# Kernel tuning notes

Hardware: AMD Instinct MI355X
Metric: run time of the kernel (lower is better)

## Reference

```python
import jax, jax.numpy as jnp
import numpy as np

B, C, D, H, W = 2, 180, 16, 32, 32
NH, WS, I = 6, 8, 2
HD = C // NH
SCALE = HD ** -0.5
N = WS ** 3                      # 512 tokens per window
TABLE = (2 * WS - 1) ** 3        # 3375 relative-position entries
HID = int(C * 4.0)               # MLP hidden
CR = C // 3                      # CAB compressed channels (compress_ratio=3)
SQ = C // 30                     # channel-attn squeeze (squeeze_factor=30)
CONV_SCALE = 0.01
EPS = 1e-5


def layer_norm(x, g, b):
    m = jnp.mean(x, axis=-1, keepdims=True)
    v = jnp.mean((x - m) ** 2, axis=-1, keepdims=True)
    return (x - m) * jax.lax.rsqrt(v + EPS) * g + b


def setup_inputs() -> dict:
    key = jax.random.key(0)
    ks = jax.random.split(key, 12)
    n = lambda i, shape: jax.random.normal(ks[i], shape, jnp.float32) * 0.02
    return {
        "x": jax.random.normal(ks[0], (B, D * H * W, C), jnp.float32),
        "x_size_d": D, "x_size_h": H, "x_size_w": W,
        "rpi_sa": jax.random.randint(ks[1], (N, N), 0, TABLE),
        "attn_mask": jnp.zeros((1,), jnp.float32),
        "triangular_masks": jnp.zeros((1,), jnp.float32),
        "g1": jnp.ones((C,), jnp.float32), "b1": jnp.zeros((C,), jnp.float32),
        "qkv_w": n(2, (3 * C, C)), "qkv_b": jnp.zeros((3 * C,), jnp.float32),
        "rpb": n(3, (TABLE, NH)),
        "proj_w": n(4, (C, C)), "proj_b": jnp.zeros((C,), jnp.float32),
        "cw1": n(5, (CR, C, 3, 3, 3)), "cb1": jnp.zeros((CR,), jnp.float32),
        "cw2": n(6, (C, CR, 3, 3, 3)), "cb2": jnp.zeros((C,), jnp.float32),
        "caw1": n(7, (SQ, C)), "cab1": jnp.zeros((SQ,), jnp.float32),
        "caw2": n(8, (C, SQ)), "cab2": jnp.zeros((C,), jnp.float32),
        "g2": jnp.ones((C,), jnp.float32), "b2": jnp.zeros((C,), jnp.float32),
        "fc1_w": n(9, (HID, C)), "fc1_b": jnp.zeros((HID,), jnp.float32),
        "fc2_w": n(10, (C, HID)), "fc2_b": jnp.zeros((C,), jnp.float32),
    }


def reference(x, x_size_d, x_size_h, x_size_w, rpi_sa, attn_mask, triangular_masks,
              g1, b1, qkv_w, qkv_b, rpb, proj_w, proj_b,
              cw1, cb1, cw2, cb2, caw1, cab1, caw2, cab2,
              g2, b2, fc1_w, fc1_b, fc2_w, fc2_b):
    Dd, Hd, Wd = x_size_d, x_size_h, x_size_w
    shortcut = x
    xn = layer_norm(x, g1, b1).reshape(B, Dd, Hd, Wd, C)

    # ---- CAB conv branch (conv3 -> gelu -> conv3 -> channel attention) ----
    xc = jnp.transpose(xn, (0, 4, 1, 2, 3))  # B C D H W
    dn = ("NCDHW", "OIDHW", "NCDHW")
    y = jax.lax.conv_general_dilated(xc, cw1, (1, 1, 1), "SAME", dimension_numbers=dn)
    y = jax.nn.gelu(y + cb1[None, :, None, None, None], approximate=False)
    y = jax.lax.conv_general_dilated(y, cw2, (1, 1, 1), "SAME", dimension_numbers=dn)
    y = y + cb2[None, :, None, None, None]
    pooled = jnp.mean(y, axis=(2, 3, 4))                      # B C (AdaptiveAvgPool3d(1))
    a = jax.nn.relu(pooled @ caw1.T + cab1)
    a = jax.nn.sigmoid(a @ caw2.T + cab2)                     # B C
    y = y * a[:, :, None, None, None]
    conv_x = jnp.transpose(y, (0, 2, 3, 4, 1)).reshape(B, Dd * Hd * Wd, C)

    # ---- sparse interval partition (interval=2, no pad, no shift) ----
    Gd, Gh, Gw = Dd // I, Hd // I, Wd // I
    xs = xn.reshape(B, Gd, I, Gh, I, Gw, I, C)
    xs = jnp.transpose(xs, (0, 2, 4, 6, 1, 3, 5, 7)).reshape(B * I ** 3, Gd, Gh, Gw, C)

    # ---- 3D window partition ----
    nd, nh, nw = Gd // WS, Gh // WS, Gw // WS
    xw = xs.reshape(-1, nd, WS, nh, WS, nw, WS, C)
    xw = jnp.transpose(xw, (0, 1, 3, 5, 2, 4, 6, 7)).reshape(-1, N, C)

    # ---- window attention with relative-position bias ----
    qkv = (xw @ qkv_w.T + qkv_b).reshape(-1, N, 3, NH, HD)
    qkv = jnp.transpose(qkv, (2, 0, 3, 1, 4))                 # 3, nWin, NH, N, HD
    q, k, v = qkv[0] * SCALE, qkv[1], qkv[2]
    attn = jnp.einsum("whnd,whmd->whnm", q, k)
    bias = rpb[rpi_sa.reshape(-1)].reshape(N, N, NH)
    attn = jax.nn.softmax(attn + jnp.transpose(bias, (2, 0, 1))[None], axis=-1)
    out = jnp.einsum("whnm,whmd->whnd", attn, v)
    out = jnp.transpose(out, (0, 2, 1, 3)).reshape(-1, N, C)
    out = out @ proj_w.T + proj_b

    # ---- window reverse + sparse reverse ----
    xs = out.reshape(-1, nd, nh, nw, WS, WS, WS, C)
    xs = jnp.transpose(xs, (0, 1, 4, 2, 5, 3, 6, 7)).reshape(B * I ** 3, Gd, Gh, Gw, C)
    xs = xs.reshape(B, I, I, I, Gd, Gh, Gw, C)
    xs = jnp.transpose(xs, (0, 4, 1, 5, 2, 6, 3, 7)).reshape(B, Dd, Hd, Wd, C)
    attn_x = xs.reshape(B, Dd * Hd * Wd, C)

    # ---- residual + conv branch, then MLP ----
    x = shortcut + attn_x + conv_x * CONV_SCALE
    h = layer_norm(x, g2, b2)
    h = jax.nn.gelu(h @ fc1_w.T + fc1_b, approximate=False) @ fc2_w.T + fc2_b
    return x + h
```

## Files before the change

### kernel.cpp

```cpp
#include <hip/hip_runtime.h>
#include <math.h>

static constexpr int CCH = 180;
static constexpr float SCALE_Q = 0.18257418583505536f;

typedef short short8 __attribute__((ext_vector_type(8)));
typedef float f32x4 __attribute__((ext_vector_type(4)));

static constexpr size_t OFF_ATTNB = 0;
static constexpr size_t OFF_XNP   = 3145728;
static constexpr size_t OFF_Y1P   = 7140864;
static constexpr size_t OFF_QKVB  = 8472576;
static constexpr size_t OFF_HID   = 0;
static constexpr size_t OFF_Y2B   = 17909760;
static constexpr size_t OFF_X2    = 21055488;
static constexpr size_t OFF_X2N   = 26953728;
static constexpr size_t OFF_BIASB = 30099456;
static constexpr size_t OFF_WQKV  = 30885888;
static constexpr size_t OFF_WPROJ = 30947328;
static constexpr size_t OFF_WFC1  = 30971904;
static constexpr size_t OFF_WFC2  = 31045632;
static constexpr size_t OFF_WB1   = 31143936;
static constexpr size_t OFF_WB2   = 31309824;
static constexpr size_t OFF_PPART = 31475712;
static constexpr size_t OFF_POOL  = 31487232;
static constexpr size_t OFF_AM    = 31487592;

__device__ __forceinline__ float geluf(float v){
  return 0.5f*v*(1.0f + erff(v*0.70710678118654752440f));
}
__device__ __forceinline__ short f2bf(float f){
  unsigned u = __float_as_uint(f);
  unsigned r = (u + 0x7FFFu + ((u>>16)&1u)) >> 16;
  return (short)r;
}
__device__ __forceinline__ float bf2f(short s){
  return __uint_as_float(((unsigned)(unsigned short)s)<<16);
}
__device__ __forceinline__ void gload16(const void* g, void* l){
  __builtin_amdgcn_global_load_lds(
    (const __attribute__((address_space(1))) unsigned int*)g,
    (__attribute__((address_space(3))) unsigned int*)l, 16, 0, 0);
}

__global__ void prep_wb(const float* __restrict__ qkv_w, const float* __restrict__ proj_w,
                        const float* __restrict__ fc1_w, const float* __restrict__ fc2_w,
                        short* __restrict__ wq, short* __restrict__ wp,
                        short* __restrict__ w1, short* __restrict__ w2){
  int i = blockIdx.x*256 + threadIdx.x;
  if(i < 122880){
    int o = i/192, k = i - o*192;
    wq[i] = (o<540 && k<180) ? f2bf(qkv_w[o*180+k]) : (short)0;
  } else if(i < 172032){
    int j = i-122880; int o = j/192, k = j - o*192;
    wp[j] = (o<180 && k<180) ? f2bf(proj_w[o*180+k]) : (short)0;
  } else if(i < 319488){
    int j = i-172032; int o = j/192, k = j - o*192;
    w1[j] = (o<720 && k<180) ? f2bf(fc1_w[o*180+k]) : (short)0;
  } else if(i < 516096){
    int j = i-319488; int o = j/768, k = j - o*768;
    w2[j] = (o<180 && k<720) ? f2bf(fc2_w[o*720+k]) : (short)0;
  }
}

__global__ void prep_wbc(const float* __restrict__ cw1, const float* __restrict__ cw2,
                         short* __restrict__ wb1, short* __restrict__ wb2){
  int i = blockIdx.x*256 + threadIdx.x;
  if(i < 27*64*192){
    int t = i/(64*192); int rem = i - t*64*192;
    int co = rem/192, ci = rem - co*192;
    wb1[i] = (co<60 && ci<180) ? f2bf(cw1[(co*180+ci)*27 + t]) : (short)0;
    int co2 = rem/64, ci2 = rem - co2*64;
    wb2[i] = (co2<180 && ci2<60) ? f2bf(cw2[(co2*60+ci2)*27 + t]) : (short)0;
  }
}

__global__ __launch_bounds__(256) void bias_prep(const int* __restrict__ rpi,
    const float* __restrict__ rpb, short* __restrict__ biasB){
  int i = blockIdx.x*256 + threadIdx.x;
  int q = i>>9, k = i&511;
  int kt = k>>5, kin = k&31;
  int j = kt*32 + ((kin<16) ? 2*kin : 2*(kin-16)+1);
  int idx = rpi[i];
  #pragma unroll
  for(int h=0;h<6;h++)
    biasB[((size_t)h*512 + q)*512 + j] = f2bf(rpb[idx*6+h]);
}

template<int PADDED>
__global__ __launch_bounds__(256) void ln_bf16(const float* __restrict__ x,
    const float* __restrict__ g, const float* __restrict__ b, short* __restrict__ outb){
  int token = blockIdx.x*4 + (threadIdx.x>>6);
  int lane  = threadIdx.x & 63;
  const float* row = x + (size_t)token*CCH;
  float v0 = row[lane], v1 = row[lane+64];
  float v2 = (lane<52) ? row[lane+128] : 0.f;
  float s = v0+v1+v2;
  #pragma unroll
  for(int m=1;m<64;m<<=1) s += __shfl_xor(s, m, 64);
  float mean = s*(1.f/180.f);
  float d0=v0-mean, d1=v1-mean, d2=(lane<52)?(v2-mean):0.f;
  float sq = d0*d0+d1*d1+d2*d2;
  #pragma unroll
  for(int m=1;m<64;m<<=1) sq += __shfl_xor(sq, m, 64);
  float rstd = rsqrtf(sq*(1.f/180.f)+1e-5f);
  size_t orow;
  if(PADDED){
    int bb=token>>14, d=(token>>10)&15, h=(token>>5)&31, w=token&31;
    orow = ((size_t)((bb*18+d+1)*34 + h+1)*34 + w+1)*192;
  } else {
    orow = (size_t)token*192;
  }
  short* o = outb + orow;
  o[lane]    = f2bf(d0*rstd*g[lane]    + b[lane]);
  o[lane+64] = f2bf(d1*rstd*g[lane+64] + b[lane+64]);
  o[lane+128]= (lane<52) ? f2bf(d2*rstd*g[lane+128] + b[lane+128]) : (short)0;
}

__global__ __launch_bounds__(256) void conv1_mfma(const short* __restrict__ in,
    const short* __restrict__ wb, const float* __restrict__ cbias, short* __restrict__ y1p){
  __shared__ short lds[26112];
  int bid = blockIdx.x;
  int xcd = bid&7, idx = bid>>3;
  int b = idx>>5, dd=(idx>>4)&1, hg=idx&15;
  int d = xcd*2+dd;
  int h0 = hg*2;
  int tid=threadIdx.x, l=tid&63, l15=l&15, g=l>>4, wid=tid>>6;
  int soff[13];
  #pragma unroll
  for(int it=0; it<13; it++){
    int t = it*256 + tid;
    int rr = t/24, s = t - rr*24;
    soff[it] = rr*192 + (((s&~7)|((s&7)^(rr&7)))<<3);
  }
  f32x4 acc[4];
  #pragma unroll
  for(int mi=0;mi<4;mi++) acc[mi]=(f32x4){0.f,0.f,0.f,0.f};
  for(int kd=0;kd<3;kd++){
    {
      const short* S = in + (((size_t)(b*18+d+kd)*34 + h0)*34)*192;
      #pragma unroll
      for(int it=0; it<13; it++){
        if(it<12 || tid<192)
          gload16(S + soff[it], &lds[(it*256 + wid*64)*8]);
      }
    }
    __syncthreads();
    #pragma unroll
    for(int kh=0;kh<3;kh++)
    #pragma unroll
    for(int kw=0;kw<3;kw++){
      const short* wt = wb + (size_t)((kd*3+kh)*3+kw)*12288 + (wid*16+l15)*192;
      #pragma unroll
      for(int ks=0;ks<6;ks++){
        int s = ks*4+g;
        short8 bv = *(const short8*)&wt[ks*32 + g*8];
        #pragma unroll
        for(int mi=0;mi<4;mi++){
          int R = ((mi>>1)+kh)*34 + (mi&1)*16 + l15 + kw;
          short8 av = *(const short8*)&lds[R*192 + (((s&~7)|((s&7)^(R&7)))<<3)];
          acc[mi] = __builtin_amdgcn_mfma_f32_16x16x32_bf16(av, bv, acc[mi],0,0,0);
        }
      }
    }
    __syncthreads();
  }
  int co = wid*16+l15;
  float bb = (co<60)? cbias[co] : 0.f;
  #pragma unroll
  for(int mi=0;mi<4;mi++){
    int hr = mi>>1;
    #pragma unroll
    for(int reg=0;reg<4;reg++){
      int r = mi*16 + g*4 + reg;
      int w = r&31;
      y1p[(((size_t)(b*18+d+1)*34 + h0+hr+1)*34 + w+1)*64 + co] = f2bf(geluf(acc[mi][reg] + bb));
    }
  }
}

__global__ __launch_bounds__(256) void conv2_mfma(const short* __restrict__ in,
    const short* __restrict__ wb, const float* __restrict__ cbias, short* __restrict__ y2b){
  __shared__ short lds[8704];
  int bid = blockIdx.x;
  int xcd = bid&7, idx = bid>>3;
  int b = idx>>5, dd=(idx>>4)&1, hg=idx&15;
  int d = xcd*2+dd;
  int h0 = hg*2;
  int tid=threadIdx.x, l=tid&63, l15=l&15, g=l>>4, wid=tid>>6;
  int soff[5];
  #pragma unroll
  for(int it=0; it<5; it++){
    int t = it*256 + tid;
    int rr = t>>3, s = t&7;
    soff[it] = rr*64 + ((s^(rr&7))<<3);
  }
  f32x4 acc[4][3];
  #pragma unroll
  for(int mi=0;mi<4;mi++)
    #pragma unroll
    for(int nj=0;nj<3;nj++) acc[mi][nj]=(f32x4){0.f,0.f,0.f,0.f};
  for(int kd=0;kd<3;kd++){
    {
      const short* S = in + (((size_t)(b*18+d+kd)*34 + h0)*34)*64;
      #pragma unroll
      for(int it=0; it<5; it++){
        if(it<4 || tid<64)
          gload16(S + soff[it], &lds[(it*256 + wid*64)*8]);
      }
    }
    __syncthreads();
    #pragma unroll
    for(int kh=0;kh<3;kh++)
    #pragma unroll
    for(int kw=0;kw<3;kw++){
      const short* wt = wb + (size_t)((kd*3+kh)*3+kw)*12288;
      #pragma unroll
      for(int ks=0;ks<2;ks++){
        int s = ks*4+g;
        short8 bv[3];
        #pragma unroll
        for(int nj=0;nj<3;nj++)
          bv[nj] = *(const short8*)&wt[(size_t)(wid*48+nj*16+l15)*64 + ks*32 + g*8];
        #pragma unroll
        for(int mi=0;mi<4;mi++){
          int R = ((mi>>1)+kh)*34 + (mi&1)*16 + l15 + kw;
          short8 av = *(const short8*)&lds[R*64 + ((s^(R&7))<<3)];
          #pragma unroll
          for(int nj=0;nj<3;nj++)
            acc[mi][nj] = __builtin_amdgcn_mfma_f32_16x16x32_bf16(av, bv[nj], acc[mi][nj],0,0,0);
        }
      }
    }
    __syncthreads();
  }
  #pragma unroll
  for(int nj=0;nj<3;nj++){
    int co = wid*48 + nj*16 + l15;
    if(co<180){
      float bb = cbias[co];
      #pragma unroll
      for(int mi=0;mi<4;mi++){
        int hr = mi>>1;
        #pragma unroll
        for(int reg=0;reg<4;reg++){
          int r = mi*16 + g*4 + reg;
          int w = r&31;
          size_t token = ((size_t)(b*16+d)*32 + h0+hr)*32 + w;
          y2b[token*192 + co] = f2bf(acc[mi][nj][reg] + bb);
        }
      }
    }
  }
}

__global__ __launch_bounds__(192) void pool1_kernel(const short* __restrict__ y2b,
                                                    float* __restrict__ part){
  int b = blockIdx.x>>5, chunk = blockIdx.x&31;
  int c = threadIdx.x;
  if(c<180){
    float s = 0.f;
    const short* base = y2b + ((size_t)b*16384 + chunk*512)*192 + c;
    for(int it=0;it<512;it++) s += bf2f(base[(size_t)it*192]);
    part[blockIdx.x*180 + c] = s;
  }
}
__global__ void pool2_kernel(const float* __restrict__ part, float* __restrict__ pooled){
  int i = blockIdx.x*256 + threadIdx.x;
  if(i<360){
    int b = i/180, c = i - b*180;
    float s = 0.f;
    for(int ch=0;ch<32;ch++) s += part[(b*32+ch)*180 + c];
    pooled[i] = s*(1.f/16384.f);
  }
}

__global__ void chattn_kernel(const float* __restrict__ pooled,
    const float* __restrict__ caw1, const float* __restrict__ cab1,
    const float* __restrict__ caw2, const float* __restrict__ cab2,
    float* __restrict__ amask){
  __shared__ float hid[2][6];
  int t = threadIdx.x;
  if(t<12){
    int b = t/6, qh = t - b*6;
    float s = cab1[qh];
    for(int c=0;c<180;c++) s += pooled[b*180+c]*caw1[qh*180+c];
    hid[b][qh] = fmaxf(s, 0.f);
  }
  __syncthreads();
  for(int i=t;i<360;i+=64){
    int b = i/180, c = i - b*180;
    float s = cab2[c];
    #pragma unroll
    for(int qh=0;qh<6;qh++) s += hid[b][qh]*caw2[c*6+qh];
    amask[i] = 1.f/(1.f+__expf(-s));
  }
}

__device__ __forceinline__ void wtok_decomp(int t, int& b, int& dd, int& hh, int& ww){
  int win = t >> 9, n = t & 511;
  int sb = win >> 2, wi = win & 3;
  int wh = wi >> 1, wwi = wi & 1;
  b = sb >> 3; int r = sb & 7;
  int id = r >> 2, ih = (r>>1)&1, iw = r&1;
  int td = n >> 6, th = (n>>3)&7, tw = n & 7;
  dd = td*2 + id;
  hh = (wh*8+th)*2 + ih;
  ww = (wwi*8+tw)*2 + iw;
}
__device__ __forceinline__ int wtok_to_row(int t){
  int b,dd,hh,ww; wtok_decomp(t,b,dd,hh,ww);
  return b*16384 + (dd*32+hh)*32 + ww;
}
__device__ __forceinline__ int wtok_to_prow(int t){
  int b,dd,hh,ww; wtok_decomp(t,b,dd,hh,ww);
  return ((b*18+dd+1)*34 + hh+1)*34 + ww + 1;
}

template<int MODE, int NOUT, int KTOT>
__global__ __launch_bounds__(256) void mgemm(const short* __restrict__ A,
    const short* __restrict__ Wb, const float* __restrict__ bias, void* __restrict__ outv,
    const float* __restrict__ e0, const float* __restrict__ e1,
    const float* __restrict__ e2){
  __shared__ short As[2][8192];
  __shared__ short Bs[2][8192];
  __shared__ int rowmap[128];
  int lin = blockIdx.y*gridDim.x + blockIdx.x;
  int xcd = lin&7, k = lin>>3;
  int bm = xcd*32 + (k & 31);
  int bn = k >> 5;
  int tid = threadIdx.x;
  int l = tid&63, l15=l&15, g=l>>4, wid=tid>>6;
  int wm = wid>>1, wn = wid&1;
  constexpr int RS = (MODE==3)?768:192;
  if(MODE==0 || MODE==1){
    if(tid<128) rowmap[tid] = (MODE==0) ? wtok_to_prow(bm*128+tid) : wtok_to_row(bm*128+tid);
  }
  __syncthreads();
  f32x4 acc[4][4];
  #pragma unroll
  for(int i=0;i<4;i++)
    #pragma unroll
    for(int j=0;j<4;j++) acc[i][j] = (f32x4){0.f,0.f,0.f,0.f};

  constexpr int NCH = KTOT/64;
  auto STAGE = [&](int ch, int p){
    int k0 = ch*64;
    #pragma unroll
    for(int it=0; it<4; it++){
      int i = it*256 + wid*64 + l;
      int r = i>>3, sl = (i&7) ^ (r&7);
      size_t row = (size_t)((MODE==0||MODE==1) ? rowmap[r] : bm*128+r);
      gload16(A + row*RS + k0 + sl*8, &As[p][(size_t)(it*256+wid*64)*8]);
    }
    #pragma unroll
    for(int it=0; it<4; it++){
      int i = it*256 + wid*64 + l;
      int c = i>>3, sl = (i&7) ^ (c&7);
      gload16(Wb + (size_t)(bn*128+c)*KTOT + k0 + sl*8, &Bs[p][(size_t)(it*256+wid*64)*8]);
    }
  };
  STAGE(0,0);
  for(int ch=0; ch<NCH; ch++){
    if(ch+1<NCH){
      STAGE(ch+1,(ch+1)&1);
      asm volatile("s_waitcnt vmcnt(8)" ::: "memory");
    } else {
      asm volatile("s_waitcnt vmcnt(0)" ::: "memory");
    }
    __builtin_amdgcn_s_barrier();
    const short* as = As[ch&1];
    const short* bs = Bs[ch&1];
    #pragma unroll
    for(int ks=0; ks<2; ks++){
      short8 av[4], bv[4];
      #pragma unroll
      for(int i=0;i<4;i++){
        int r = wm*64 + i*16 + l15;
        av[i] = *(const short8*)&as[r*64 + (((ks*4+g) ^ (r&7))<<3)];
      }
      #pragma unroll
      for(int j=0;j<4;j++){
        int c = wn*64 + j*16 + l15;
        bv[j] = *(const short8*)&bs[c*64 + (((ks*4+g) ^ (c&7))<<3)];
      }
      #pragma unroll
      for(int i=0;i<4;i++)
        #pragma unroll
        for(int j=0;j<4;j++)
          acc[i][j] = __builtin_amdgcn_mfma_f32_16x16x32_bf16(av[i], bv[j], acc[i][j],0,0,0);
    }
    asm volatile("" ::: "memory");
    __builtin_amdgcn_s_barrier();
  }
  #pragma unroll
  for(int i=0;i<4;i++){
    int rloc0 = wm*64 + i*16 + g*4;
    #pragma unroll
    for(int j=0;j<4;j++){
      int o = bn*128 + wn*64 + j*16 + l15;
      if(MODE!=2 && o>=NOUT) continue;
      float bb = (o<NOUT) ? bias[o] : 0.f;
      #pragma unroll
      for(int reg=0; reg<4; reg++){
        int rl = rloc0 + reg;
        int trow = bm*128 + rl;
        float v = acc[i][j][reg] + bb;
        if(MODE==0){
          int which = o/180; int chn = o - which*180;
          int head = chn/30; int hd = chn - head*30;
          int win = trow>>9, n = trow&511;
          if(which==0){
            size_t sidx = ((size_t)(win*6+head)*512 + n)*32;
            ((short*)outv)[sidx + hd] = f2bf(v*SCALE_Q);
            if(hd==0) *(int*)&((short*)outv)[sidx + 30] = 0;
          } else if(which==1){
            size_t sidx = 6291456 + ((size_t)(win*6+head)*512 + n)*32;
            ((short*)outv)[sidx + hd] = f2bf(v);
            if(hd==0) *(int*)&((short*)outv)[sidx + 30] = 0;
          } else {
            ((short*)outv)[12582912 + ((size_t)(win*6+head)*32 + hd)*512 + n] = f2bf(v);
          }
        } else if(MODE==1){
          int grow = rowmap[rl];
          float conv = bf2f(((const short*)e1)[(size_t)grow*192 + o]);
          float am   = e2[(grow>>14)*180 + o];
          ((float*)outv)[(size_t)grow*180+o] = v + e0[(size_t)grow*180+o] + conv*am*0.01f;
        } else if(MODE==2){
          ((short*)outv)[(size_t)trow*768+o] = (o<720) ? f2bf(geluf(v)) : (short)0;
        } else {
          ((float*)outv)[(size_t)trow*180+o] = v + e0[(size_t)trow*180+o];
        }
      }
    }
  }
}

__global__ __launch_bounds__(256) void attn_mfma(const short* __restrict__ qkvb,
    const short* __restrict__ biasB, short* __restrict__ attnb){
  __shared__ short Ks[1024];
  __shared__ short Vt[1024];
  __shared__ short Ps[4096];
  int bid = blockIdx.x;
  int j0 = bid>>3;
  int grp = (bid&7)*48 + (j0>>2);
  int qt = j0&3;
  int win = grp/6, head = grp - (grp/6)*6;
  int tid = threadIdx.x, w = tid>>6, l = tid&63, l15 = l&15, g = l>>4;
  const short* qp = qkvb + (size_t)(win*6+head)*16384;
  const short* kp = qp + 6291456;
  const short* vp = qkvb + 12582912 + (size_t)(win*6+head)*16384;
  int qbase = qt*128 + w*32;
  short8 aq0 = *(const short8*)&qp[(size_t)(qbase + l15)*32 + g*8];
  short8 aq1 = *(const short8*)&qp[(size_t)(qbase + 16 + l15)*32 + g*8];
  const short* bB = biasB + ((size_t)head*512 + qbase)*512;
  f32x4 acc[2][2];
  float lsum[2][4];
  #pragma unroll
  for(int a=0;a<2;a++){
    #pragma unroll
    for(int r=0;r<4;r++) lsum[a][r]=0.f;
    #pragma unroll
    for(int b2=0;b2<2;b2++) acc[a][b2]=(f32x4){0.f,0.f,0.f,0.f};
  }
  int pbase = w*1024;
  int rrA = l15>>1, sA = ((l15&1)<<2)|g;
  int offT0 = rrA*64 + ((sA ^ (rrA&7))<<3);
  int rrB = 8+rrA;
  int offT1 = rrB*64 + ((sA ^ (rrB&7))<<3);
  int strr = (tid&127)>>3, sts = tid&7;
  int stoff = strr*64 + ((sts ^ (strr&7))<<3);
  int sttok = strr*2 + (sts>>2), sthd8 = (sts&3)*8;

  for(int kt=0; kt<16; kt++){
    if(tid<128){
      short8 v = *(const short8*)&kp[(size_t)(kt*32+sttok)*32 + sthd8];
      *(short8*)&Ks[stoff] = v;
    } else {
      short8 v = *(const short8*)&vp[(size_t)sttok*512 + kt*32 + sthd8];
      *(short8*)&Vt[stoff] = v;
    }
    unsigned ub[2][4];
    #pragma unroll
    for(int mf=0; mf<2; mf++)
      #pragma unroll
      for(int reg=0; reg<4; reg++)
        ub[mf][reg] = *(const unsigned*)&bB[(size_t)(mf*16+g*4+reg)*512 + kt*32 + 2*l15];
    __syncthreads();
    short8 bk0 = *(const short8*)&Ks[offT0];
    short8 bk1 = *(const short8*)&Ks[offT1];
    f32x4 z = (f32x4){0.f,0.f,0.f,0.f};
    f32x4 s00 = __builtin_amdgcn_mfma_f32_16x16x32_bf16(aq0, bk0, z,0,0,0);
    f32x4 s01 = __builtin_amdgcn_mfma_f32_16x16x32_bf16(aq0, bk1, z,0,0,0);
    f32x4 s10 = __builtin_amdgcn_mfma_f32_16x16x32_bf16(aq1, bk0, z,0,0,0);
    f32x4 s11 = __builtin_amdgcn_mfma_f32_16x16x32_bf16(aq1, bk1, z,0,0,0);
    #pragma unroll
    for(int mf=0; mf<2; mf++){
      #pragma unroll
      for(int reg=0; reg<4; reg++){
        float b0 = __uint_as_float(ub[mf][reg]<<16);
        float b1 = __uint_as_float(ub[mf][reg]&0xFFFF0000u);
        float sv0 = (mf==0)? s00[reg] : s10[reg];
        float sv1 = (mf==0)? s01[reg] : s11[reg];
        float p0 = __expf(fminf(sv0 + b0, 60.f));
        float p1 = __expf(fminf(sv1 + b1, 60.f));
        lsum[mf][reg] += p0 + p1;
        int q = mf*16 + g*4 + reg;
        int rr = q>>1;
        int s0 = ((q&1)<<2) | (l15>>3);
        int s1 = s0 + 2;
        Ps[pbase + rr*64 + ((s0 ^ (rr&7))<<3) + (l15&7)] = f2bf(p0);
        Ps[pbase + rr*64 + ((s1 ^ (rr&7))<<3) + (l15&7)] = f2bf(p1);
      }
    }
    short8 ap0 = *(const short8*)&Ps[pbase + offT0];
    short8 ap1 = *(const short8*)&Ps[pbase + offT1];
    short8 bv0 = *(const short8*)&Vt[offT0];
    short8 bv1 = *(const short8*)&Vt[offT1];
    acc[0][0] = __builtin_amdgcn_mfma_f32_16x16x32_bf16(ap0, bv0, acc[0][0],0,0,0);
    acc[0][1] = __builtin_amdgcn_mfma_f32_16x16x32_bf16(ap0, bv1, acc[0][1],0,0,0);
    acc[1][0] = __builtin_amdgcn_mfma_f32_16x16x32_bf16(ap1, bv0, acc[1][0],0,0,0);
    acc[1][1] = __builtin_amdgcn_mfma_f32_16x16x32_bf16(ap1, bv1, acc[1][1],0,0,0);
    __syncthreads();
  }
  int token = win*512 + qbase;
  #pragma unroll
  for(int mf=0; mf<2; mf++)
  #pragma unroll
  for(int reg=0; reg<4; reg++){
    float lv = lsum[mf][reg];
    lv += __shfl_xor(lv,1,64); lv += __shfl_xor(lv,2,64);
    lv += __shfl_xor(lv,4,64); lv += __shfl_xor(lv,8,64);
    float inv = 1.f/lv;
    int qg = token + mf*16 + g*4 + reg;
    short* orow = attnb + (size_t)qg*192 + head*30;
    if(l15<30) orow[l15] = f2bf(acc[mf][0][reg]*inv);
    if(l15<14) orow[16+l15] = f2bf(acc[mf][1][reg]*inv);
    if(head==5 && l15<12) attnb[(size_t)qg*192 + 180 + l15] = 0;
  }
}

extern "C" void kernel_launch(void* const* d_in, const int* in_sizes, int n_in,
                              void* d_out, int out_size, void* d_ws, size_t ws_size,
                              hipStream_t stream){
  const float* x      = (const float*)d_in[0];
  const int*   rpi    = (const int*)  d_in[4];
  const float* g1     = (const float*)d_in[7];
  const float* b1     = (const float*)d_in[8];
  const float* qkv_w  = (const float*)d_in[9];
  const float* qkv_b  = (const float*)d_in[10];
  const float* rpb    = (const float*)d_in[11];
  const float* proj_w = (const float*)d_in[12];
  const float* proj_b = (const float*)d_in[13];
  const float* cw1    = (const float*)d_in[14];
  const float* cb1    = (const float*)d_in[15];
  const float* cw2    = (const float*)d_in[16];
  const float* cb2    = (const float*)d_in[17];
  const float* caw1   = (const float*)d_in[18];
  const float* cab1   = (const float*)d_in[19];
  const float* caw2   = (const float*)d_in[20];
  const float* cab2   = (const float*)d_in[21];
  const float* g2     = (const float*)d_in[22];
  const float* b2     = (const float*)d_in[23];
  const float* fc1_w  = (const float*)d_in[24];
  const float* fc1_b  = (const float*)d_in[25];
  const float* fc2_w  = (const float*)d_in[26];
  const float* fc2_b  = (const float*)d_in[27];
  float* ws = (float*)d_ws;
  float* fout = (float*)d_out;
  short* attnb = (short*)(ws + OFF_ATTNB);
  short* xnp   = (short*)(ws + OFF_XNP);
  short* y1p   = (short*)(ws + OFF_Y1P);
  short* qkvb  = (short*)(ws + OFF_QKVB);
  short* hid   = (short*)(ws + OFF_HID);
  short* y2b   = (short*)(ws + OFF_Y2B);
  short* x2n   = (short*)(ws + OFF_X2N);
  short* biasB = (short*)(ws + OFF_BIASB);
  short* wq    = (short*)(ws + OFF_WQKV);
  short* wp    = (short*)(ws + OFF_WPROJ);
  short* w1    = (short*)(ws + OFF_WFC1);
  short* w2    = (short*)(ws + OFF_WFC2);
  short* wb1   = (short*)(ws + OFF_WB1);
  short* wb2   = (short*)(ws + OFF_WB2);

  hipMemsetAsync(xnp, 0, (size_t)7990272*2, stream);
  hipMemsetAsync(y1p, 0, (size_t)2663424*2, stream);
  prep_wb<<<2016,256,0,stream>>>(qkv_w, proj_w, fc1_w, fc2_w, wq, wp, w1, w2);
  prep_wbc<<<1296,256,0,stream>>>(cw1, cw2, wb1, wb2);
  bias_prep<<<1024,256,0,stream>>>(rpi, rpb, biasB);
  ln_bf16<1><<<8192,256,0,stream>>>(x, g1, b1, xnp);
  conv1_mfma<<<512,256,0,stream>>>(xnp, wb1, cb1, y1p);
  conv2_mfma<<<512,256,0,stream>>>(y1p, wb2, cb2, y2b);
  pool1_kernel<<<64,192,0,stream>>>(y2b, ws+OFF_PPART);
  pool2_kernel<<<2,256,0,stream>>>(ws+OFF_PPART, ws+OFF_POOL);
  chattn_kernel<<<1,64,0,stream>>>(ws+OFF_POOL, caw1, cab1, caw2, cab2, ws+OFF_AM);
  mgemm<0,540,192><<<dim3(256,5),256,0,stream>>>(
      xnp, wq, qkv_b, qkvb, nullptr, nullptr, nullptr);
  attn_mfma<<<1536,256,0,stream>>>(qkvb, biasB, attnb);
  mgemm<1,180,192><<<dim3(256,2),256,0,stream>>>(
      attnb, wp, proj_b, ws+OFF_X2, x, (const float*)y2b, ws+OFF_AM);
  ln_bf16<0><<<8192,256,0,stream>>>(ws+OFF_X2, g2, b2, x2n);
  mgemm<2,720,192><<<dim3(256,6),256,0,stream>>>(
      x2n, w1, fc1_b, hid, nullptr, nullptr, nullptr);
  mgemm<3,180,768><<<dim3(256,2),256,0,stream>>>(
      hid, w2, fc2_b, fout, ws+OFF_X2, nullptr, nullptr);
}
```

Before: 456.0 us.

## Restructure conv kernels to stage all depth slices and fuse channel pooling

conv1 now loads all three depth slices into LDS at once (about 156KB) and splits the 27 kernel taps across the four waves. Each wave computes all 64 output channels, and the partial sums are reduced through LDS before GELU and the store. conv2 also preloads all three slices, removing the per-slice barriers. It fuses the global average pool by having each block atomically add its per-channel sums, so the two pool kernels go away. The conv2 bias is folded into the channel-attention input, at the cost of one LDS-heavy block per CU and float atomics that make the sums order-nondeterministic.

```diff
diff --git a/kernel.cpp b/kernel.cpp
--- a/kernel.cpp
+++ b/kernel.cpp
@@ -22,9 +22,8 @@
 static constexpr size_t OFF_WFC2  = 31045632;
 static constexpr size_t OFF_WB1   = 31143936;
 static constexpr size_t OFF_WB2   = 31309824;
-static constexpr size_t OFF_PPART = 31475712;
-static constexpr size_t OFF_POOL  = 31487232;
-static constexpr size_t OFF_AM    = 31487592;
+static constexpr size_t OFF_POOL  = 31475712;
+static constexpr size_t OFF_AM    = 31476072;
 
 __device__ __forceinline__ float geluf(float v){
   return 0.5f*v*(1.0f + erff(v*0.70710678118654752440f));
@@ -117,8 +116,84 @@
   o[lane+128]= (lane<52) ? f2bf(d2*rstd*g[lane+128] + b[lane+128]) : (short)0;
 }
 
-__global__ __launch_bounds__(256) void conv1_mfma(const short* __restrict__ in,
+__global__ __launch_bounds__(256,1) void conv1_mfma(const short* __restrict__ in,
     const short* __restrict__ wb, const float* __restrict__ cbias, short* __restrict__ y1p){
+  __shared__ short lds[78336];
+  int bid = blockIdx.x;
+  int xcd = bid&7, idx = bid>>3;
+  int b = idx>>5, dd=(idx>>4)&1, hg=idx&15;
+  int d = xcd*2+dd;
+  int h0 = hg*2;
+  int tid=threadIdx.x, l=tid&63, l15=l&15, g=l>>4, wid=tid>>6;
+  int soff[13];
+  #pragma unroll
+  for(int it=0; it<13; it++){
+    int t = it*256 + tid;
+    int rr = t/24, s = t - rr*24;
+    soff[it] = rr*192 + (((s&~7)|((s&7)^(rr&7)))<<3);
+  }
+  #pragma unroll
+  for(int kd=0; kd<3; kd++){
+    const short* S = in + (((size_t)(b*18+d+kd)*34 + h0)*34)*192;
+    short* L = lds + kd*26112;
+    #pragma unroll
+    for(int it=0; it<13; it++){
+      if(it<12 || tid<192)
+        gload16(S + soff[it], L + (size_t)(it*256+wid*64)*8);
+    }
+  }
+  asm volatile("s_waitcnt vmcnt(0)" ::: "memory");
+  __builtin_amdgcn_s_barrier();
+  f32x4 acc[4][4];
+  #pragma unroll
+  for(int i=0;i<4;i++)
+    #pragma unroll
+    for(int j=0;j<4;j++) acc[i][j]=(f32x4){0.f,0.f,0.f,0.f};
+  for(int ti = wid; ti < 27; ti += 4){
+    int kd = ti/9; int r2 = ti - kd*9; int kh = r2/3; int kw = r2 - kh*3;
+    const short* wt = wb + (size_t)ti*12288;
+    int Rb = kd*136 + kh*34 + kw;
+    #pragma unroll
+    for(int ks=0; ks<6; ks++){
+      int s = ks*4+g;
+      short8 bv[4];
+      #pragma unroll
+      for(int nj=0;nj<4;nj++)
+        bv[nj] = *(const short8*)&wt[(size_t)(nj*16+l15)*192 + ks*32 + g*8];
+      #pragma unroll
+      for(int mi=0;mi<4;mi++){
+        int R = Rb + (mi>>1)*34 + (mi&1)*16 + l15;
+        short8 av = *(const short8*)&lds[R*192 + (((s&~7)|((s&7)^(R&7)))<<3)];
+        #pragma unroll
+        for(int nj=0;nj<4;nj++)
+          acc[mi][nj] = __builtin_amdgcn_mfma_f32_16x16x32_bf16(av, bv[nj], acc[mi][nj],0,0,0);
+      }
+    }
+  }
+  __syncthreads();
+  float* scrf = (float*)lds;
+  #pragma unroll
+  for(int i=0;i<4;i++)
+    #pragma unroll
+    for(int j=0;j<4;j++)
+      #pragma unroll
+      for(int reg=0;reg<4;reg++)
+        scrf[wid*4160 + (i*16+g*4+reg)*65 + j*16+l15] = acc[i][j][reg];
+  __syncthreads();
+  size_t prow0 = ((size_t)(b*18+d+1)*34 + h0+1)*34 + 1;
+  for(int idx2=tid; idx2<4096; idx2+=256){
+    int r = idx2>>6, co = idx2&63;
+    float v = scrf[r*65+co] + scrf[4160 + r*65+co]
+            + scrf[8320 + r*65+co] + scrf[12480 + r*65+co];
+    float bb = (co<60)? cbias[co] : 0.f;
+    int hr = r>>5, w = r&31;
+    y1p[(prow0 + hr*34 + w)*64 + co] = f2bf(geluf(v+bb));
+  }
+}
+
+__global__ __launch_bounds__(256) void conv2_mfma(const short* __restrict__ in,
+    const short* __restrict__ wb, const float* __restrict__ cbias,
+    short* __restrict__ y2b, float* __restrict__ pooled){
   __shared__ short lds[26112];
   int bid = blockIdx.x;
   int xcd = bid&7, idx = bid>>3;
@@ -126,68 +201,6 @@
   int d = xcd*2+dd;
   int h0 = hg*2;
   int tid=threadIdx.x, l=tid&63, l15=l&15, g=l>>4, wid=tid>>6;
-  int soff[13];
-  #pragma unroll
-  for(int it=0; it<13; it++){
-    int t = it*256 + tid;
-    int rr = t/24, s = t - rr*24;
-    soff[it] = rr*192 + (((s&~7)|((s&7)^(rr&7)))<<3);
-  }
-  f32x4 acc[4];
-  #pragma unroll
-  for(int mi=0;mi<4;mi++) acc[mi]=(f32x4){0.f,0.f,0.f,0.f};
-  for(int kd=0;kd<3;kd++){
-    {
-      const short* S = in + (((size_t)(b*18+d+kd)*34 + h0)*34)*192;
-      #pragma unroll
-      for(int it=0; it<13; it++){
-        if(it<12 || tid<192)
-          gload16(S + soff[it], &lds[(it*256 + wid*64)*8]);
-      }
-    }
-    __syncthreads();
-    #pragma unroll
-    for(int kh=0;kh<3;kh++)
-    #pragma unroll
-    for(int kw=0;kw<3;kw++){
-      const short* wt = wb + (size_t)((kd*3+kh)*3+kw)*12288 + (wid*16+l15)*192;
-      #pragma unroll
-      for(int ks=0;ks<6;ks++){
-        int s = ks*4+g;
-        short8 bv = *(const short8*)&wt[ks*32 + g*8];
-        #pragma unroll
-        for(int mi=0;mi<4;mi++){
-          int R = ((mi>>1)+kh)*34 + (mi&1)*16 + l15 + kw;
-          short8 av = *(const short8*)&lds[R*192 + (((s&~7)|((s&7)^(R&7)))<<3)];
-          acc[mi] = __builtin_amdgcn_mfma_f32_16x16x32_bf16(av, bv, acc[mi],0,0,0);
-        }
-      }
-    }
-    __syncthreads();
-  }
-  int co = wid*16+l15;
-  float bb = (co<60)? cbias[co] : 0.f;
-  #pragma unroll
-  for(int mi=0;mi<4;mi++){
-    int hr = mi>>1;
-    #pragma unroll
-    for(int reg=0;reg<4;reg++){
-      int r = mi*16 + g*4 + reg;
-      int w = r&31;
-      y1p[(((size_t)(b*18+d+1)*34 + h0+hr+1)*34 + w+1)*64 + co] = f2bf(geluf(acc[mi][reg] + bb));
-    }
-  }
-}
-
-__global__ __launch_bounds__(256) void conv2_mfma(const short* __restrict__ in,
-    const short* __restrict__ wb, const float* __restrict__ cbias, short* __restrict__ y2b){
-  __shared__ short lds[8704];
-  int bid = blockIdx.x;
-  int xcd = bid&7, idx = bid>>3;
-  int b = idx>>5, dd=(idx>>4)&1, hg=idx&15;
-  int d = xcd*2+dd;
-  int h0 = hg*2;
-  int tid=threadIdx.x, l=tid&63, l15=l&15, g=l>>4, wid=tid>>6;
   int soff[5];
   #pragma unroll
   for(int it=0; it<5; it++){
@@ -195,87 +208,71 @@
     int rr = t>>3, s = t&7;
     soff[it] = rr*64 + ((s^(rr&7))<<3);
   }
+  #pragma unroll
+  for(int kd=0; kd<3; kd++){
+    const short* S = in + (((size_t)(b*18+d+kd)*34 + h0)*34)*64;
+    short* L = lds + kd*8704;
+    #pragma unroll
+    for(int it=0; it<5; it++){
+      if(it<4 || tid<64)
+        gload16(S + soff[it], L + (size_t)(it*256+wid*64)*8);
+    }
+  }
+  asm volatile("s_waitcnt vmcnt(0)" ::: "memory");
+  __builtin_amdgcn_s_barrier();
   f32x4 acc[4][3];
   #pragma unroll
   for(int mi=0;mi<4;mi++)
     #pragma unroll
     for(int nj=0;nj<3;nj++) acc[mi][nj]=(f32x4){0.f,0.f,0.f,0.f};
-  for(int kd=0;kd<3;kd++){
-    {
-      const short* S = in + (((size_t)(b*18+d+kd)*34 + h0)*34)*64;
-      #pragma unroll
-      for(int it=0; it<5; it++){
-        if(it<4 || tid<64)
-          gload16(S + soff[it], &lds[(it*256 + wid*64)*8]);
-      }
-    }
-    __syncthreads();
-    #pragma unroll
-    for(int kh=0;kh<3;kh++)
-    #pragma unroll
-    for(int kw=0;kw<3;kw++){
-      const short* wt = wb + (size_t)((kd*3+kh)*3+kw)*12288;
-      #pragma unroll
-      for(int ks=0;ks<2;ks++){
-        int s = ks*4+g;
-        short8 bv[3];
+  for(int ti=0; ti<27; ti++){
+    int kd = ti/9; int r2 = ti - kd*9; int kh = r2/3; int kw = r2 - kh*3;
+    const short* wt = wb + (size_t)ti*12288;
+    int Rb = kd*136 + kh*34 + kw;
+    #pragma unroll
+    for(int ks=0; ks<2; ks++){
+      int s = ks*4+g;
+      short8 bv[3];
+      #pragma unroll
+      for(int nj=0;nj<3;nj++)
+        bv[nj] = *(const short8*)&wt[(size_t)(wid*48+nj*16+l15)*64 + ks*32 + g*8];
+      #pragma unroll
+      for(int mi=0;mi<4;mi++){
+        int R = Rb + (mi>>1)*34 + (mi&1)*16 + l15;
+        short8 av = *(const short8*)&lds[R*64 + ((s^(R&7))<<3)];
         #pragma unroll
         for(int nj=0;nj<3;nj++)
-          bv[nj] = *(const short8*)&wt[(size_t)(wid*48+nj*16+l15)*64 + ks*32 + g*8];
-        #pragma unroll
-        for(int mi=0;mi<4;mi++){
-          int R = ((mi>>1)+kh)*34 + (mi&1)*16 + l15 + kw;
-          short8 av = *(const short8*)&lds[R*64 + ((s^(R&7))<<3)];
-          #pragma unroll
-          for(int nj=0;nj<3;nj++)
-            acc[mi][nj] = __builtin_amdgcn_mfma_f32_16x16x32_bf16(av, bv[nj], acc[mi][nj],0,0,0);
-        }
+          acc[mi][nj] = __builtin_amdgcn_mfma_f32_16x16x32_bf16(av, bv[nj], acc[mi][nj],0,0,0);
       }
     }
-    __syncthreads();
-  }
+  }
+  size_t token0 = ((size_t)(b*16+d)*32 + h0)*32;
   #pragma unroll
   for(int nj=0;nj<3;nj++){
     int co = wid*48 + nj*16 + l15;
+    float ps = 0.f;
+    #pragma unroll
+    for(int mi=0;mi<4;mi++)
+      #pragma unroll
+      for(int reg=0;reg<4;reg++) ps += acc[mi][nj][reg];
+    ps += __shfl_xor(ps,16,64);
+    ps += __shfl_xor(ps,32,64);
     if(co<180){
       float bb = cbias[co];
       #pragma unroll
-      for(int mi=0;mi<4;mi++){
-        int hr = mi>>1;
+      for(int mi=0;mi<4;mi++)
         #pragma unroll
         for(int reg=0;reg<4;reg++){
           int r = mi*16 + g*4 + reg;
-          int w = r&31;
-          size_t token = ((size_t)(b*16+d)*32 + h0+hr)*32 + w;
-          y2b[token*192 + co] = f2bf(acc[mi][nj][reg] + bb);
+          int hr = r>>5, w = r&31;
+          y2b[(token0 + hr*32 + w)*192 + co] = f2bf(acc[mi][nj][reg] + bb);
         }
-      }
-    }
-  }
-}
-
-__global__ __launch_bounds__(192) void pool1_kernel(const short* __restrict__ y2b,
-                                                    float* __restrict__ part){
-  int b = blockIdx.x>>5, chunk = blockIdx.x&31;
-  int c = threadIdx.x;
-  if(c<180){
-    float s = 0.f;
-    const short* base = y2b + ((size_t)b*16384 + chunk*512)*192 + c;
-    for(int it=0;it<512;it++) s += bf2f(base[(size_t)it*192]);
-    part[blockIdx.x*180 + c] = s;
-  }
-}
-__global__ void pool2_kernel(const float* __restrict__ part, float* __restrict__ pooled){
-  int i = blockIdx.x*256 + threadIdx.x;
-  if(i<360){
-    int b = i/180, c = i - b*180;
-    float s = 0.f;
-    for(int ch=0;ch<32;ch++) s += part[(b*32+ch)*180 + c];
-    pooled[i] = s*(1.f/16384.f);
-  }
-}
-
-__global__ void chattn_kernel(const float* __restrict__ pooled,
+      if(l<16) atomicAdd(&pooled[b*180 + co], ps);
+    }
+  }
+}
+
+__global__ void chattn_kernel(const float* __restrict__ pooled, const float* __restrict__ cb2,
     const float* __restrict__ caw1, const float* __restrict__ cab1,
     const float* __restrict__ caw2, const float* __restrict__ cab2,
     float* __restrict__ amask){
@@ -284,7 +281,10 @@
   if(t<12){
     int b = t/6, qh = t - b*6;
     float s = cab1[qh];
-    for(int c=0;c<180;c++) s += pooled[b*180+c]*caw1[qh*180+c];
+    for(int c=0;c<180;c++){
+      float pv = pooled[b*180+c]*(1.f/16384.f) + cb2[c];
+      s += pv*caw1[qh*180+c];
+    }
     hid[b][qh] = fmaxf(s, 0.f);
   }
   __syncthreads();
@@ -585,15 +585,14 @@
 
   hipMemsetAsync(xnp, 0, (size_t)7990272*2, stream);
   hipMemsetAsync(y1p, 0, (size_t)2663424*2, stream);
+  hipMemsetAsync(ws+OFF_POOL, 0, 360*4, stream);
   prep_wb<<<2016,256,0,stream>>>(qkv_w, proj_w, fc1_w, fc2_w, wq, wp, w1, w2);
   prep_wbc<<<1296,256,0,stream>>>(cw1, cw2, wb1, wb2);
   bias_prep<<<1024,256,0,stream>>>(rpi, rpb, biasB);
   ln_bf16<1><<<8192,256,0,stream>>>(x, g1, b1, xnp);
   conv1_mfma<<<512,256,0,stream>>>(xnp, wb1, cb1, y1p);
-  conv2_mfma<<<512,256,0,stream>>>(y1p, wb2, cb2, y2b);
-  pool1_kernel<<<64,192,0,stream>>>(y2b, ws+OFF_PPART);
-  pool2_kernel<<<2,256,0,stream>>>(ws+OFF_PPART, ws+OFF_POOL);
-  chattn_kernel<<<1,64,0,stream>>>(ws+OFF_POOL, caw1, cab1, caw2, cab2, ws+OFF_AM);
+  conv2_mfma<<<512,256,0,stream>>>(y1p, wb2, cb2, y2b, ws+OFF_POOL);
+  chattn_kernel<<<1,64,0,stream>>>(ws+OFF_POOL, cb2, caw1, cab1, caw2, cab2, ws+OFF_AM);
   mgemm<0,540,192><<<dim3(256,5),256,0,stream>>>(
       xnp, wq, qkv_b, qkvb, nullptr, nullptr, nullptr);
   attn_mfma<<<1536,256,0,stream>>>(qkvb, biasB, attnb);
```

After: 448.5 us. Within noise of the previous version (-1.6%).
